# Kernel tuning notes

Hardware: AMD Instinct MI355X
Metric: run time of the kernel (lower is better)

Reference implementation:

```python
import jax, jax.numpy as jnp
import numpy as np

B, T, N, D = 1, 128, 32768, 1024


def setup_inputs() -> dict:
    key = jax.random.key(0)
    k1, k2 = jax.random.split(key)
    inputs = jax.random.normal(k1, (B, N, D), dtype=jnp.float32)
    # Nested tag->token coverage: tag i covers tokens [i*s, N). This guarantees
    # each tag keeps s exclusive tokens after the 'direct string' deduction,
    # so the row-normalization never divides by zero (matches real DOM data).
    s = N // T
    tok = jnp.arange(N)
    ttt = (tok[None, :] >= (jnp.arange(T) * s)[:, None]).astype(jnp.float32)  # (T, N)
    tag_to_token = jnp.broadcast_to(ttt[None], (B, T, N)).astype(jnp.float32)
    # Tag adjacency: self-loops + sparse random children.
    rand = jax.random.bernoulli(k2, 0.05, (T, T))
    gat_mask = (jnp.eye(T, dtype=bool) | rand).astype(jnp.int32)[None]  # (B, T, T)
    return {"inputs": inputs, "tag_to_token": tag_to_token, "gat_mask": gat_mask}


def deduce_direct_string(tag_to_token):
    # temp[i] = binary[i] - sum_{j>i} binary[j]  (original loop reads unmodified suffix rows)
    binary = (tag_to_token > 0).astype(tag_to_token.dtype)
    suffix_incl = jnp.flip(jnp.cumsum(jnp.flip(binary, axis=1), axis=1), axis=1)
    temp = binary - (suffix_incl - binary)
    temp = jnp.where(temp > 0, temp, 0.0)
    return temp / jnp.sum(temp, axis=2, keepdims=True)


def deduce_child(gat_mask):
    # Faithful to the torch nested loop (valid for B == 1).
    L = gat_mask.shape[1]

    def outer(i, child):
        child = child.at[:, i].set(gat_mask[:, i])

        def inner(j, c):
            temp = c[:, j][:, None, :] * gat_mask[:, j][:, None, :]  # (B,1,L)
            return ((c - temp) > 0).astype(c.dtype)

        return jax.lax.fori_loop(i + 1, L, inner, child)

    return jax.lax.fori_loop(0, L, outer, jnp.zeros_like(gat_mask))


def reference(inputs, tag_to_token, gat_mask):
    gm = gat_mask.astype(inputs.dtype)
    t2t = deduce_direct_string(tag_to_token)          # (B, T, N)
    child = deduce_child(gm)                          # (B, T, T)
    outputs = jnp.matmul(t2t, inputs)                 # (B, T, D)
    Tn = outputs.shape[1]

    # Triangular recurrence, i = T-1 ... 0; row i reads already-updated rows > i.
    def step(o, i):
        row = jnp.einsum('bt,btd->bd', child[:, i], o)
        return o.at[:, i].set(row), None

    outputs, _ = jax.lax.scan(step, outputs, jnp.arange(Tn - 1, -1, -1))
    return outputs
```

## Files before the change

kernel.cpp:

```cpp
#include <hip/hip_runtime.h>

#define NTOK 32768
#define NTAG 128
#define DDIM 1024
#define TPB 128


__global__ __launch_bounds__(256) void k_zero(const int* __restrict__ gm,
                                              float* __restrict__ P,
                                              int* __restrict__ cnt,
                                              unsigned* __restrict__ maskT) {
    const int tid = threadIdx.x;
    const int gid = blockIdx.x * 256 + tid;
    reinterpret_cast<float4*>(P)[gid] = make_float4(0.f, 0.f, 0.f, 0.f);
    if (gid < NTAG) cnt[gid] = 0;

    if (blockIdx.x == 1 || blockIdx.x == 2) {
        const int idx = (blockIdx.x - 1) * 256 + tid;
        const int l = idx & 15;
        const int iw = (idx >> 4) & 3;
        const int k = idx >> 6;
        const int colg = 16 * k + l;
        unsigned w = 0;
#pragma unroll
        for (int ib = 0; ib < 32; ++ib)
            w |= (unsigned)(gm[(iw * 32 + ib) * NTAG + colg] != 0) << ib;
        maskT[idx] = w;
    }
}

__global__ __launch_bounds__(256, 1) void k_fused(const float* __restrict__ inp,
                                                  const float* __restrict__ t2t,
                                                  float* __restrict__ P,
                                                  int* __restrict__ cnt) {
    __shared__ int part[2][TPB];
    __shared__ int tags[TPB];
    const int tid = threadIdx.x;
    const int n0 = blockIdx.x * TPB;

    {
        const int c = tid >> 7;
        const int n = tid & 127;
        int m = -1;
#pragma unroll
        for (int j = 0; j < 64; ++j) {
            const int r = c * 64 + j;
            if (t2t[(size_t)r * NTOK + n0 + n] > 0.f) m = r;
        }
        part[c][n] = m;
    }
    __syncthreads();
    if (tid < TPB) tags[tid] = max(part[0][tid], part[1][tid]);
    __syncthreads();

    const int col = tid * 4;
    const float4* src = reinterpret_cast<const float4*>(inp) + (size_t)n0 * 256 + tid;

    float4 acc = make_float4(0.f, 0.f, 0.f, 0.f);
    int cur = tags[0];
    int runlen = 0;

#pragma unroll
    for (int gr = 0; gr < 8; ++gr) {
        float4 v[16];
#pragma unroll
        for (int k = 0; k < 16; ++k)
            v[k] = src[(size_t)(gr * 16 + k) * 256];
#pragma unroll
        for (int k = 0; k < 16; ++k) {
            const int tg = tags[gr * 16 + k];
            if (tg != cur) {
                if (cur >= 0) {
                    float* p = P + (size_t)cur * DDIM + col;
                    atomicAdd(p + 0, acc.x);
                    atomicAdd(p + 1, acc.y);
                    atomicAdd(p + 2, acc.z);
                    atomicAdd(p + 3, acc.w);
                    if (tid == 0) atomicAdd(&cnt[cur], runlen);
                }
                acc = make_float4(0.f, 0.f, 0.f, 0.f);
                cur = tg;
                runlen = 0;
            }
            if (tg >= 0) {
                acc.x += v[k].x;
                acc.y += v[k].y;
                acc.z += v[k].z;
                acc.w += v[k].w;
                ++runlen;
            }
        }
    }
    if (cur >= 0) {
        float* p = P + (size_t)cur * DDIM + col;
        atomicAdd(p + 0, acc.x);
        atomicAdd(p + 1, acc.y);
        atomicAdd(p + 2, acc.z);
        atomicAdd(p + 3, acc.w);
        if (tid == 0) atomicAdd(&cnt[cur], runlen);
    }
}

template <int CTRL>
__device__ __forceinline__ float dpp_add(float x) {
    const int y = __builtin_amdgcn_update_dpp(0, __float_as_int(x), CTRL, 0xF, 0xF, true);
    return x + __int_as_float(y);
}

__global__ __launch_bounds__(64, 1) void k_recur(const float* __restrict__ P,
                                                 const unsigned* __restrict__ maskT,
                                                 const int* __restrict__ cnt,
                                                 float* __restrict__ out) {
    __shared__ float xpose[NTAG][5];
    const int L = threadIdx.x;
    const int g = L >> 4;
    const int l = L & 15;
    const int c0 = blockIdx.x * 4;

    unsigned mw[8][4];
#pragma unroll
    for (int k = 0; k < 8; ++k)
#pragma unroll
        for (int iw = 0; iw < 4; ++iw) mw[k][iw] = maskT[(k * 4 + iw) * 16 + l];

    const float ia = 1.0f / (float)cnt[L];
    const float ib_ = 1.0f / (float)cnt[64 + L];
    float4 pa = *reinterpret_cast<const float4*>(P + (size_t)L * DDIM + c0);
    float4 pb = *reinterpret_cast<const float4*>(P + (size_t)(64 + L) * DDIM + c0);
    xpose[L][0] = pa.x * ia;
    xpose[L][1] = pa.y * ia;
    xpose[L][2] = pa.z * ia;
    xpose[L][3] = pa.w * ia;
    xpose[64 + L][0] = pb.x * ib_;
    xpose[64 + L][1] = pb.y * ib_;
    xpose[64 + L][2] = pb.z * ib_;
    xpose[64 + L][3] = pb.w * ib_;
    __syncthreads();

    float o0 = xpose[l][g], o1 = xpose[16 + l][g];
    float o2 = xpose[32 + l][g], o3 = xpose[48 + l][g];
    float o4 = xpose[64 + l][g], o5 = xpose[80 + l][g];
    float o6 = xpose[96 + l][g], o7 = xpose[112 + l][g];

#define SECTION(IW, KU, IBHI, IBLO)                                         \
    _Pragma("unroll 2") for (int ib = IBHI; ib >= IBLO; --ib) {             \
        float sa = (float)((mw[0][IW] >> ib) & 1u) * o0;                    \
        sa += (float)((mw[1][IW] >> ib) & 1u) * o1;                         \
        sa += (float)((mw[2][IW] >> ib) & 1u) * o2;                         \
        sa += (float)((mw[3][IW] >> ib) & 1u) * o3;                         \
        float sb = (float)((mw[4][IW] >> ib) & 1u) * o4;                    \
        sb += (float)((mw[5][IW] >> ib) & 1u) * o5;                         \
        sb += (float)((mw[6][IW] >> ib) & 1u) * o6;                         \
        sb += (float)((mw[7][IW] >> ib) & 1u) * o7;                         \
        float s = sa + sb;                                                  \
        s = dpp_add<0xB1>(s);                                               \
        s = dpp_add<0x4E>(s);                                               \
        s = dpp_add<0x141>(s);                                              \
        s = dpp_add<0x140>(s);                                              \
        if (l == (ib & 15)) o##KU = s;                                      \
    }

    SECTION(3, 7, 31, 16)
    SECTION(3, 6, 15, 0)
    SECTION(2, 5, 31, 16)
    SECTION(2, 4, 15, 0)
    SECTION(1, 3, 31, 16)
    SECTION(1, 2, 15, 0)
    SECTION(0, 1, 31, 16)
    SECTION(0, 0, 15, 0)
#undef SECTION

    __syncthreads();
    xpose[l][g] = o0;
    xpose[16 + l][g] = o1;
    xpose[32 + l][g] = o2;
    xpose[48 + l][g] = o3;
    xpose[64 + l][g] = o4;
    xpose[80 + l][g] = o5;
    xpose[96 + l][g] = o6;
    xpose[112 + l][g] = o7;
    __syncthreads();
    float4 ra, rb;
    ra.x = xpose[L][0];
    ra.y = xpose[L][1];
    ra.z = xpose[L][2];
    ra.w = xpose[L][3];
    rb.x = xpose[64 + L][0];
    rb.y = xpose[64 + L][1];
    rb.z = xpose[64 + L][2];
    rb.w = xpose[64 + L][3];
    *reinterpret_cast<float4*>(out + (size_t)L * DDIM + c0) = ra;
    *reinterpret_cast<float4*>(out + (size_t)(64 + L) * DDIM + c0) = rb;
}

extern "C" void kernel_launch(void* const* d_in, const int* in_sizes, int n_in,
                              void* d_out, int out_size, void* d_ws, size_t ws_size,
                              hipStream_t stream) {
    const float* inp = (const float*)d_in[0];
    const float* t2t = (const float*)d_in[1];
    const int* gm = (const int*)d_in[2];
    float* out = (float*)d_out;

    char* ws = (char*)d_ws;
    float* P = (float*)ws;
    int* cnt = (int*)(ws + 524288);
    unsigned* maskT = (unsigned*)(ws + 524800);

    k_zero<<<128, 256, 0, stream>>>(gm, P, cnt, maskT);
    k_fused<<<NTOK / TPB, 256, 0, stream>>>(inp, t2t, P, cnt);
    k_recur<<<DDIM / 4, 64, 0, stream>>>(P, maskT, cnt, out);
}
```

Measured before the change: 45.82 us.

## Merge three kernels into one cooperative kernel with grid-wide syncs

Replaces the zero, fused-accumulate and recurrence kernels with a single cooperative launch of 256 blocks that separates the phases with grid.sync(). The recurrence phase now runs on 64 blocks of four wavefronts each, with a separate shared transpose buffer per wavefront. The aim is to remove two kernel launch gaps and their host-side launch cost. In exchange it pays for two grid-wide barriers, and the final phase uses only a quarter of the blocks while the rest sit idle.

```diff
diff --git a/kernel.cpp b/kernel.cpp
--- a/kernel.cpp
+++ b/kernel.cpp
@@ -1,105 +1,13 @@
 #include <hip/hip_runtime.h>
+#include <hip/hip_cooperative_groups.h>
+
+namespace cg = cooperative_groups;
 
 #define NTOK 32768
 #define NTAG 128
 #define DDIM 1024
 #define TPB 128
 
-
-__global__ __launch_bounds__(256) void k_zero(const int* __restrict__ gm,
-                                              float* __restrict__ P,
-                                              int* __restrict__ cnt,
-                                              unsigned* __restrict__ maskT) {
-    const int tid = threadIdx.x;
-    const int gid = blockIdx.x * 256 + tid;
-    reinterpret_cast<float4*>(P)[gid] = make_float4(0.f, 0.f, 0.f, 0.f);
-    if (gid < NTAG) cnt[gid] = 0;
-
-    if (blockIdx.x == 1 || blockIdx.x == 2) {
-        const int idx = (blockIdx.x - 1) * 256 + tid;
-        const int l = idx & 15;
-        const int iw = (idx >> 4) & 3;
-        const int k = idx >> 6;
-        const int colg = 16 * k + l;
-        unsigned w = 0;
-#pragma unroll
-        for (int ib = 0; ib < 32; ++ib)
-            w |= (unsigned)(gm[(iw * 32 + ib) * NTAG + colg] != 0) << ib;
-        maskT[idx] = w;
-    }
-}
-
-__global__ __launch_bounds__(256, 1) void k_fused(const float* __restrict__ inp,
-                                                  const float* __restrict__ t2t,
-                                                  float* __restrict__ P,
-                                                  int* __restrict__ cnt) {
-    __shared__ int part[2][TPB];
-    __shared__ int tags[TPB];
-    const int tid = threadIdx.x;
-    const int n0 = blockIdx.x * TPB;
-
-    {
-        const int c = tid >> 7;
-        const int n = tid & 127;
-        int m = -1;
-#pragma unroll
-        for (int j = 0; j < 64; ++j) {
-            const int r = c * 64 + j;
-            if (t2t[(size_t)r * NTOK + n0 + n] > 0.f) m = r;
-        }
-        part[c][n] = m;
-    }
-    __syncthreads();
-    if (tid < TPB) tags[tid] = max(part[0][tid], part[1][tid]);
-    __syncthreads();
-
-    const int col = tid * 4;
-    const float4* src = reinterpret_cast<const float4*>(inp) + (size_t)n0 * 256 + tid;
-
-    float4 acc = make_float4(0.f, 0.f, 0.f, 0.f);
-    int cur = tags[0];
-    int runlen = 0;
-
-#pragma unroll
-    for (int gr = 0; gr < 8; ++gr) {
-        float4 v[16];
-#pragma unroll
-        for (int k = 0; k < 16; ++k)
-            v[k] = src[(size_t)(gr * 16 + k) * 256];
-#pragma unroll
-        for (int k = 0; k < 16; ++k) {
-            const int tg = tags[gr * 16 + k];
-            if (tg != cur) {
-                if (cur >= 0) {
-                    float* p = P + (size_t)cur * DDIM + col;
-                    atomicAdd(p + 0, acc.x);
-                    atomicAdd(p + 1, acc.y);
-                    atomicAdd(p + 2, acc.z);
-                    atomicAdd(p + 3, acc.w);
-                    if (tid == 0) atomicAdd(&cnt[cur], runlen);
-                }
-                acc = make_float4(0.f, 0.f, 0.f, 0.f);
-                cur = tg;
-                runlen = 0;
-            }
-            if (tg >= 0) {
-                acc.x += v[k].x;
-                acc.y += v[k].y;
-                acc.z += v[k].z;
-                acc.w += v[k].w;
-                ++runlen;
-            }
-        }
-    }
-    if (cur >= 0) {
-        float* p = P + (size_t)cur * DDIM + col;
-        atomicAdd(p + 0, acc.x);
-        atomicAdd(p + 1, acc.y);
-        atomicAdd(p + 2, acc.z);
-        atomicAdd(p + 3, acc.w);
-        if (tid == 0) atomicAdd(&cnt[cur], runlen);
-    }
-}
 
 template <int CTRL>
 __device__ __forceinline__ float dpp_add(float x) {
@@ -107,40 +15,138 @@
     return x + __int_as_float(y);
 }
 
-__global__ __launch_bounds__(64, 1) void k_recur(const float* __restrict__ P,
-                                                 const unsigned* __restrict__ maskT,
-                                                 const int* __restrict__ cnt,
-                                                 float* __restrict__ out) {
-    __shared__ float xpose[NTAG][5];
-    const int L = threadIdx.x;
-    const int g = L >> 4;
-    const int l = L & 15;
-    const int c0 = blockIdx.x * 4;
-
-    unsigned mw[8][4];
-#pragma unroll
-    for (int k = 0; k < 8; ++k)
-#pragma unroll
-        for (int iw = 0; iw < 4; ++iw) mw[k][iw] = maskT[(k * 4 + iw) * 16 + l];
-
-    const float ia = 1.0f / (float)cnt[L];
-    const float ib_ = 1.0f / (float)cnt[64 + L];
-    float4 pa = *reinterpret_cast<const float4*>(P + (size_t)L * DDIM + c0);
-    float4 pb = *reinterpret_cast<const float4*>(P + (size_t)(64 + L) * DDIM + c0);
-    xpose[L][0] = pa.x * ia;
-    xpose[L][1] = pa.y * ia;
-    xpose[L][2] = pa.z * ia;
-    xpose[L][3] = pa.w * ia;
-    xpose[64 + L][0] = pb.x * ib_;
-    xpose[64 + L][1] = pb.y * ib_;
-    xpose[64 + L][2] = pb.z * ib_;
-    xpose[64 + L][3] = pb.w * ib_;
-    __syncthreads();
-
-    float o0 = xpose[l][g], o1 = xpose[16 + l][g];
-    float o2 = xpose[32 + l][g], o3 = xpose[48 + l][g];
-    float o4 = xpose[64 + l][g], o5 = xpose[80 + l][g];
-    float o6 = xpose[96 + l][g], o7 = xpose[112 + l][g];
+__global__ __launch_bounds__(256, 1) void k_all(const float* __restrict__ inp,
+                                                const float* __restrict__ t2t,
+                                                const int* __restrict__ gm,
+                                                float* __restrict__ P,
+                                                int* __restrict__ cnt,
+                                                unsigned* __restrict__ maskT,
+                                                float* __restrict__ out) {
+    cg::grid_group grid = cg::this_grid();
+    __shared__ int part[2][TPB];
+    __shared__ int tags[TPB];
+    __shared__ float xpose[4][NTAG][5];
+    const int tid = threadIdx.x;
+    const int bid = blockIdx.x;
+
+    {
+        const int gid = bid * 256 + tid;
+        if (gid < 32768) reinterpret_cast<float4*>(P)[gid] = make_float4(0.f, 0.f, 0.f, 0.f);
+        if (gid < NTAG) cnt[gid] = 0;
+        if (bid == 1 || bid == 2) {
+            const int idx = (bid - 1) * 256 + tid;
+            const int l = idx & 15;
+            const int iw = (idx >> 4) & 3;
+            const int k = idx >> 6;
+            const int colg = 16 * k + l;
+            unsigned w = 0;
+#pragma unroll
+            for (int ib = 0; ib < 32; ++ib)
+                w |= (unsigned)(gm[(iw * 32 + ib) * NTAG + colg] != 0) << ib;
+            maskT[idx] = w;
+        }
+    }
+    grid.sync();
+
+    {
+        const int n0 = bid * TPB;
+        {
+            const int c = tid >> 7;
+            const int n = tid & 127;
+            int m = -1;
+#pragma unroll
+            for (int j = 0; j < 64; ++j) {
+                const int r = c * 64 + j;
+                if (t2t[(size_t)r * NTOK + n0 + n] > 0.f) m = r;
+            }
+            part[c][n] = m;
+        }
+        __syncthreads();
+        if (tid < TPB) tags[tid] = max(part[0][tid], part[1][tid]);
+        __syncthreads();
+
+        const int col = tid * 4;
+        const float4* src =
+            reinterpret_cast<const float4*>(inp) + (size_t)n0 * 256 + tid;
+
+        float4 acc = make_float4(0.f, 0.f, 0.f, 0.f);
+        int cur = tags[0];
+        int runlen = 0;
+
+#pragma unroll
+        for (int gr = 0; gr < 8; ++gr) {
+            float4 v[16];
+#pragma unroll
+            for (int k = 0; k < 16; ++k)
+                v[k] = src[(size_t)(gr * 16 + k) * 256];
+#pragma unroll
+            for (int k = 0; k < 16; ++k) {
+                const int tg = tags[gr * 16 + k];
+                if (tg != cur) {
+                    if (cur >= 0) {
+                        float* p = P + (size_t)cur * DDIM + col;
+                        atomicAdd(p + 0, acc.x);
+                        atomicAdd(p + 1, acc.y);
+                        atomicAdd(p + 2, acc.z);
+                        atomicAdd(p + 3, acc.w);
+                        if (tid == 0) atomicAdd(&cnt[cur], runlen);
+                    }
+                    acc = make_float4(0.f, 0.f, 0.f, 0.f);
+                    cur = tg;
+                    runlen = 0;
+                }
+                if (tg >= 0) {
+                    acc.x += v[k].x;
+                    acc.y += v[k].y;
+                    acc.z += v[k].z;
+                    acc.w += v[k].w;
+                    ++runlen;
+                }
+            }
+        }
+        if (cur >= 0) {
+            float* p = P + (size_t)cur * DDIM + col;
+            atomicAdd(p + 0, acc.x);
+            atomicAdd(p + 1, acc.y);
+            atomicAdd(p + 2, acc.z);
+            atomicAdd(p + 3, acc.w);
+            if (tid == 0) atomicAdd(&cnt[cur], runlen);
+        }
+    }
+    grid.sync();
+
+    if (bid < 64) {
+        const int wv = tid >> 6;
+        const int L = tid & 63;
+        const int g = L >> 4;
+        const int l = L & 15;
+        const int c0 = bid * 16 + wv * 4;
+        float(*xp)[5] = xpose[wv];
+
+        unsigned mw[8][4];
+#pragma unroll
+        for (int k = 0; k < 8; ++k)
+#pragma unroll
+            for (int iw = 0; iw < 4; ++iw) mw[k][iw] = maskT[(k * 4 + iw) * 16 + l];
+
+        const float ia = 1.0f / (float)cnt[L];
+        const float ib_ = 1.0f / (float)cnt[64 + L];
+        float4 pa = *reinterpret_cast<const float4*>(P + (size_t)L * DDIM + c0);
+        float4 pb = *reinterpret_cast<const float4*>(P + (size_t)(64 + L) * DDIM + c0);
+        xp[L][0] = pa.x * ia;
+        xp[L][1] = pa.y * ia;
+        xp[L][2] = pa.z * ia;
+        xp[L][3] = pa.w * ia;
+        xp[64 + L][0] = pb.x * ib_;
+        xp[64 + L][1] = pb.y * ib_;
+        xp[64 + L][2] = pb.z * ib_;
+        xp[64 + L][3] = pb.w * ib_;
+        __syncthreads();
+
+        float o0 = xp[l][g], o1 = xp[16 + l][g];
+        float o2 = xp[32 + l][g], o3 = xp[48 + l][g];
+        float o4 = xp[64 + l][g], o5 = xp[80 + l][g];
+        float o6 = xp[96 + l][g], o7 = xp[112 + l][g];
 
 #define SECTION(IW, KU, IBHI, IBLO)                                         \
     _Pragma("unroll 2") for (int ib = IBHI; ib >= IBLO; --ib) {             \
@@ -160,37 +166,38 @@
         if (l == (ib & 15)) o##KU = s;                                      \
     }
 
-    SECTION(3, 7, 31, 16)
-    SECTION(3, 6, 15, 0)
-    SECTION(2, 5, 31, 16)
-    SECTION(2, 4, 15, 0)
-    SECTION(1, 3, 31, 16)
-    SECTION(1, 2, 15, 0)
-    SECTION(0, 1, 31, 16)
-    SECTION(0, 0, 15, 0)
+        SECTION(3, 7, 31, 16)
+        SECTION(3, 6, 15, 0)
+        SECTION(2, 5, 31, 16)
+        SECTION(2, 4, 15, 0)
+        SECTION(1, 3, 31, 16)
+        SECTION(1, 2, 15, 0)
+        SECTION(0, 1, 31, 16)
+        SECTION(0, 0, 15, 0)
 #undef SECTION
 
-    __syncthreads();
-    xpose[l][g] = o0;
-    xpose[16 + l][g] = o1;
-    xpose[32 + l][g] = o2;
-    xpose[48 + l][g] = o3;
-    xpose[64 + l][g] = o4;
-    xpose[80 + l][g] = o5;
-    xpose[96 + l][g] = o6;
-    xpose[112 + l][g] = o7;
-    __syncthreads();
-    float4 ra, rb;
-    ra.x = xpose[L][0];
-    ra.y = xpose[L][1];
-    ra.z = xpose[L][2];
-    ra.w = xpose[L][3];
-    rb.x = xpose[64 + L][0];
-    rb.y = xpose[64 + L][1];
-    rb.z = xpose[64 + L][2];
-    rb.w = xpose[64 + L][3];
-    *reinterpret_cast<float4*>(out + (size_t)L * DDIM + c0) = ra;
-    *reinterpret_cast<float4*>(out + (size_t)(64 + L) * DDIM + c0) = rb;
+        __syncthreads();
+        xp[l][g] = o0;
+        xp[16 + l][g] = o1;
+        xp[32 + l][g] = o2;
+        xp[48 + l][g] = o3;
+        xp[64 + l][g] = o4;
+        xp[80 + l][g] = o5;
+        xp[96 + l][g] = o6;
+        xp[112 + l][g] = o7;
+        __syncthreads();
+        float4 ra, rb;
+        ra.x = xp[L][0];
+        ra.y = xp[L][1];
+        ra.z = xp[L][2];
+        ra.w = xp[L][3];
+        rb.x = xp[64 + L][0];
+        rb.y = xp[64 + L][1];
+        rb.z = xp[64 + L][2];
+        rb.w = xp[64 + L][3];
+        *reinterpret_cast<float4*>(out + (size_t)L * DDIM + c0) = ra;
+        *reinterpret_cast<float4*>(out + (size_t)(64 + L) * DDIM + c0) = rb;
+    }
 }
 
 extern "C" void kernel_launch(void* const* d_in, const int* in_sizes, int n_in,
@@ -206,7 +213,7 @@
     int* cnt = (int*)(ws + 524288);
     unsigned* maskT = (unsigned*)(ws + 524800);
 
-    k_zero<<<128, 256, 0, stream>>>(gm, P, cnt, maskT);
-    k_fused<<<NTOK / TPB, 256, 0, stream>>>(inp, t2t, P, cnt);
-    k_recur<<<DDIM / 4, 64, 0, stream>>>(P, maskT, cnt, out);
+    void* args[] = {(void*)&inp, (void*)&t2t, (void*)&gm, (void*)&P,
+                    (void*)&cnt, (void*)&maskT, (void*)&out};
+    hipLaunchCooperativeKernel((void*)k_all, dim3(256), dim3(256), args, 0, stream);
 }
```

Result: slower. 107.7 us (+135.0%).
